# Kernel tuning notes

Measured on AMD Instinct MI355X. Metric: run time of the kernel, lower is better.

Reference implementation:

```python
import jax, jax.numpy as jnp
import numpy as np

N_NODES = 100000
NODES_PER_GRAPH = 200
N_GRAPHS = N_NODES // NODES_PER_GRAPH  # 500
N_EDGES = 3200000
NUM_FEATURES = 128
HIDDEN = 32
K_POOL = 50
NUM_CLASSES = 10
NUM_ITERATIONS = 3


def setup_inputs() -> dict:
    key = jax.random.key(0)
    ks = jax.random.split(key, 12)
    x = jax.random.normal(ks[0], (N_NODES, NUM_FEATURES), dtype=jnp.float32)
    edge_index = jax.random.randint(ks[1], (2, N_EDGES), 0, N_NODES, dtype=jnp.int64)
    batch = (jnp.arange(N_NODES, dtype=jnp.int64) // NODES_PER_GRAPH)
    # GCN weights (glorot-ish scale) + biases
    W1 = jax.random.normal(ks[2], (NUM_FEATURES, HIDDEN), dtype=jnp.float32) * (1.0 / np.sqrt(NUM_FEATURES))
    b1 = jnp.zeros((HIDDEN,), dtype=jnp.float32)
    W2 = jax.random.normal(ks[3], (HIDDEN, HIDDEN), dtype=jnp.float32) * (1.0 / np.sqrt(HIDDEN))
    b2 = jnp.zeros((HIDDEN,), dtype=jnp.float32)
    W3 = jax.random.normal(ks[4], (HIDDEN, HIDDEN), dtype=jnp.float32) * (1.0 / np.sqrt(HIDDEN))
    b3 = jnp.zeros((HIDDEN,), dtype=jnp.float32)
    # Capsule weights: [out_capsules, in_capsules, out_length, in_length]
    Wc1 = jax.random.normal(ks[5], (16, K_POOL, 32, 3 * HIDDEN), dtype=jnp.float32) * 0.05
    Wc2 = jax.random.normal(ks[6], (NUM_CLASSES, 16, 16, 32), dtype=jnp.float32) * 0.05
    return {"x": x, "edge_index": edge_index, "batch": batch,
            "W1": W1, "b1": b1, "W2": W2, "b2": b2, "W3": W3, "b3": b3,
            "Wc1": Wc1, "Wc2": Wc2}


def _gcn_conv(x, W, b, src, dst, mask):
    # PyG GCNConv: remove self-loops already done (mask), add self-loops, sym-normalize.
    h = x @ W  # [N, H]
    deg = jnp.zeros((x.shape[0],), dtype=h.dtype).at[dst].add(mask) + 1.0  # self-loop adds 1
    dinv = jax.lax.rsqrt(deg)
    norm = dinv[src] * dinv[dst] * mask  # [E]
    agg = jnp.zeros_like(h).at[dst].add(norm[:, None] * h[src])
    agg = agg + h * (dinv * dinv)[:, None]  # self-loop contribution h_i / deg_i
    return agg + b


def _squash(s, axis=-1):
    sq = jnp.sum(s * s, axis=axis, keepdims=True)
    return (sq / (1.0 + sq)) * s * jax.lax.rsqrt(sq + 1e-12)


def _capsule_linear(u, W, num_iterations):
    # u: [B, I, in_len]; W: [O, I, out_len, in_len]
    priors = jnp.einsum('oiLl,bil->boiL', W, u)  # [B, O, I, out_len]
    logits = jnp.zeros(priors.shape[:3] + (1,), dtype=priors.dtype)
    for it in range(num_iterations):
        c = jax.nn.softmax(logits, axis=1)             # over out capsules
        s = jnp.sum(c * priors, axis=2)                # [B, O, out_len]
        v = _squash(s)
        if it < num_iterations - 1:
            logits = logits + jnp.sum(priors * v[:, :, None, :], axis=-1, keepdims=True)
    return v


def _global_sort_pool(x, k):
    # x: [N, C], equal-size graphs -> [B, nper, C]; sort desc by last channel, take top-k
    xg = x.reshape(N_GRAPHS, NODES_PER_GRAPH, x.shape[-1])
    order = jnp.argsort(-xg[:, :, -1], axis=1)[:, :k]  # [B, k]
    return jnp.take_along_axis(xg, order[:, :, None], axis=1)  # [B, k, C]


def reference(x, edge_index, batch, W1, b1, W2, b2, W3, b3, Wc1, Wc2):
    src, dst = edge_index[0], edge_index[1]
    mask = (src != dst).astype(x.dtype)  # remove_self_loops
    x1 = jnp.tanh(_gcn_conv(x, W1, b1, src, dst, mask))
    x2 = jnp.tanh(_gcn_conv(x1, W2, b2, src, dst, mask))
    x3 = jnp.tanh(_gcn_conv(x2, W3, b3, src, dst, mask))
    xc = jnp.concatenate([x1, x2, x3], axis=-1)        # [N, 96]
    pooled = _global_sort_pool(xc, K_POOL)             # [B, 50, 96]
    out = _capsule_linear(pooled, Wc1, NUM_ITERATIONS)  # [B, 16, 32]
    out = _capsule_linear(out, Wc2, NUM_ITERATIONS)     # [B, 10, 16]
    return jnp.linalg.norm(out, axis=-1)                # [B, 10]
```

## Files before the change

kernel.cpp:

```cpp
#include <hip/hip_runtime.h>

#define NNODES 100000
#define NEDGES 3200000
#define NPG 200
#define NGRAPH 500
#define FIN 128
#define HID 32
#define KP 50
#define NCLS 10

#define NB1 196
#define BSH 9
#define CHUNK 8192
#define NBLK1 391
#define CAP 17408

__global__ __launch_bounds__(512) void k_place1(const int* __restrict__ src,
                                                const int* __restrict__ dst,
                                                int* __restrict__ cursor,
                                                unsigned* __restrict__ csorted) {
    __shared__ int hist[NB1];
    __shared__ int lstart[NB1];
    __shared__ int base[NB1];
    __shared__ int cnt2[NB1];
    __shared__ int sarr[256];
    __shared__ unsigned buf[CHUNK];
    __shared__ int dbuf[CHUNK];
    int t = threadIdx.x;
    for (int i = t; i < NB1; i += 512) { hist[i] = 0; cnt2[i] = 0; }
    __syncthreads();
    int eb = blockIdx.x * CHUNK;
    for (int i = 0; i < CHUNK / 512; ++i) {
        int e = eb + t + i * 512;
        if (e < NEDGES) {
            int s = src[e], d = dst[e];
            if (s != d) atomicAdd(&hist[d >> BSH], 1);
        }
    }
    __syncthreads();
    if (t < 256) sarr[t] = (t < NB1) ? hist[t] : 0;
    __syncthreads();
    for (int ofs = 1; ofs < 256; ofs <<= 1) {
        int add = (t < 256 && t >= ofs) ? sarr[t - ofs] : 0;
        __syncthreads();
        if (t < 256) sarr[t] += add;
        __syncthreads();
    }
    if (t < NB1) {
        lstart[t] = (t == 0) ? 0 : sarr[t - 1];
        base[t] = hist[t] ? (t * CAP + atomicAdd(&cursor[t], hist[t])) : 0;
    }
    __syncthreads();
    for (int i = 0; i < CHUNK / 512; ++i) {
        int e = eb + t + i * 512;
        if (e < NEDGES) {
            int s = src[e], d = dst[e];
            if (s != d) {
                int bk = d >> BSH;
                int pos = atomicAdd(&cnt2[bk], 1);
                int slot = lstart[bk] + pos;
                buf[slot] = ((unsigned)s << BSH) | (unsigned)(d & 511);
                dbuf[slot] = base[bk] + pos;
            }
        }
    }
    __syncthreads();
    int nval = sarr[NB1 - 1];
    for (int j = t; j < nval; j += 512) csorted[dbuf[j]] = buf[j];
}

__global__ __launch_bounds__(512) void k_fill2(const int* __restrict__ cursor,
                                               const unsigned* __restrict__ csorted,
                                               int* __restrict__ csrc,
                                               int2* __restrict__ begend,
                                               float* __restrict__ dinv) {
    __shared__ int cnt[512];
    __shared__ int loffs[512];
    __shared__ int cnt2[512];
    __shared__ int sarr[512];
    int b = blockIdx.x, t = threadIdx.x;
    cnt[t] = 0; cnt2[t] = 0;
    __syncthreads();
    int base = b * CAP;
    int m = cursor[b];
    for (int j = t; j < m; j += 512) atomicAdd(&cnt[csorted[base + j] & 511], 1);
    __syncthreads();
    sarr[t] = cnt[t];
    __syncthreads();
    for (int ofs = 1; ofs < 512; ofs <<= 1) {
        int add = (t >= ofs) ? sarr[t - ofs] : 0;
        __syncthreads();
        sarr[t] += add;
        __syncthreads();
    }
    loffs[t] = sarr[t] - cnt[t];
    __syncthreads();
    int n = b * 512 + t;
    if (n < NNODES) {
        int beg = base + loffs[t];
        begend[n] = make_int2(beg, beg + cnt[t]);
        dinv[n] = rsqrtf((float)cnt[t] + 1.0f);
    }
    for (int j = t; j < m; j += 512) {
        unsigned p = csorted[base + j];
        int d = p & 511;
        int pos = atomicAdd(&cnt2[d], 1);
        csrc[base + loffs[d] + pos] = (int)(p >> BSH);
    }
}

__global__ __launch_bounds__(256) void k_matmul(const float* __restrict__ X, int ldx, int K,
                                                const float* __restrict__ W,
                                                const float* __restrict__ dinv,
                                                float* __restrict__ h) {
    __shared__ float Xl[64 * FIN];
    __shared__ float Wqf[(FIN / 4) * 128];
    int t = threadIdx.x;
    for (int idx = t; idx < K * HID; idx += 256) {
        int k = idx >> 5, j = idx & 31;
        Wqf[(k >> 2) * 128 + j * 4 + (k & 3)] = W[idx];
    }
    int n0 = blockIdx.x * 64;
    int ng = 64 * K / 4;
    for (int idx = t; idx < ng; idx += 256) {
        int r = (idx * 4) / K, c = (idx * 4) % K;
        float4 v = make_float4(0.f, 0.f, 0.f, 0.f);
        if (n0 + r < NNODES)
            v = *reinterpret_cast<const float4*>(X + (size_t)(n0 + r) * ldx + c);
        *reinterpret_cast<float4*>(&Xl[r * K + c]) = v;
    }
    __syncthreads();
    int j = t & 31, g = t >> 5;
    const float* xr = &Xl[(g * 8) * K];
    const float4* wq = reinterpret_cast<const float4*>(Wqf);
    float a[8] = {0, 0, 0, 0, 0, 0, 0, 0};
    int K4 = K >> 2;
    for (int k4 = 0; k4 < K4; ++k4) {
        float4 wv = wq[k4 * 32 + j];
#pragma unroll
        for (int r = 0; r < 8; ++r) {
            float4 xv = *reinterpret_cast<const float4*>(&xr[r * K + k4 * 4]);
            a[r] += xv.x * wv.x + xv.y * wv.y + xv.z * wv.z + xv.w * wv.w;
        }
    }
    int r0 = n0 + g * 8;
#pragma unroll
    for (int q = 0; q < 8; ++q)
        if (r0 + q < NNODES) h[(size_t)(r0 + q) * HID + j] = a[q] * dinv[r0 + q];
}

__global__ __launch_bounds__(256) void k_gather(const int2* __restrict__ begend,
                                                const int* __restrict__ csrc,
                                                const float* __restrict__ dinv,
                                                const float* __restrict__ hw,
                                                const float* __restrict__ bias,
                                                float* __restrict__ xc, int coloff) {
    int t = threadIdx.x;
    int wv = t >> 6;
    int lane = t & 63;
    int nh = lane >> 5;
    int sub = lane & 31;
    int g = sub >> 3;
    int q = sub & 7;
    int n = blockIdx.x * 8 + wv * 2 + nh;
    int2 be = begend[n];
    int beg = be.x, end = be.y, last = end - 1;
    float4 acc = make_float4(0.f, 0.f, 0.f, 0.f);
    for (int e0 = beg + g; e0 < end; e0 += 32) {
#pragma unroll
        for (int j = 0; j < 8; ++j) {
            int e = e0 + 4 * j;
            float mk = (e <= last) ? 1.f : 0.f;
            int s = csrc[min(e, last)];
            float4 hv = *reinterpret_cast<const float4*>(hw + (size_t)s * HID + q * 4);
            acc.x += mk * hv.x; acc.y += mk * hv.y; acc.z += mk * hv.z; acc.w += mk * hv.w;
        }
    }
    for (int m = 8; m <= 16; m <<= 1) {
        acc.x += __shfl_xor(acc.x, m, 64);
        acc.y += __shfl_xor(acc.y, m, 64);
        acc.z += __shfl_xor(acc.z, m, 64);
        acc.w += __shfl_xor(acc.w, m, 64);
    }
    if (g == 0) {
        float di = dinv[n];
        float4 hv = *reinterpret_cast<const float4*>(hw + (size_t)n * HID + q * 4);
        float4 bv = *reinterpret_cast<const float4*>(bias + q * 4);
        float4 v;
        v.x = tanhf(di * (acc.x + hv.x) + bv.x);
        v.y = tanhf(di * (acc.y + hv.y) + bv.y);
        v.z = tanhf(di * (acc.z + hv.z) + bv.z);
        v.w = tanhf(di * (acc.w + hv.w) + bv.w);
        *reinterpret_cast<float4*>(xc + (size_t)n * 96 + coloff + q * 4) = v;
    }
}

__global__ __launch_bounds__(256) void k_sortpool(const float* __restrict__ xc,
                                                  float* __restrict__ pooled) {
    int g = blockIdx.x;
    __shared__ float vals[NPG];
    __shared__ int sel[KP];
    int t = threadIdx.x;
    if (t < NPG) vals[t] = xc[((size_t)g * NPG + t) * 96 + 95];
    __syncthreads();
    if (t < NPG) {
        float v = vals[t];
        int r = 0;
        for (int k = 0; k < NPG; ++k) {
            float vk = vals[k];
            r += (vk > v) || (vk == v && k < t);
        }
        if (r < KP) sel[r] = t;
    }
    __syncthreads();
    for (int idx = t; idx < KP * 24; idx += 256) {
        int r = idx / 24, c4 = (idx % 24) * 4;
        *reinterpret_cast<float4*>(pooled + (size_t)g * KP * 96 + r * 96 + c4) =
            *reinterpret_cast<const float4*>(xc + ((size_t)g * NPG + sel[r]) * 96 + c4);
    }
}

__global__ __launch_bounds__(512, 2) void k_priors1(const float* __restrict__ pooled,
                                                    const float* __restrict__ Wc1,
                                                    float* __restrict__ priors) {
    int bid = blockIdx.x;
    int ct = bid & 3;
    int bt = (bid >> 2) & 1;
    int i = bid >> 3;
    __shared__ float As[48 * 256];
    __shared__ float Bs[48 * 128];
    int t = threadIdx.x;
    int tx = t & 15, ty = t >> 4;
    float acc[8][8];
#pragma unroll
    for (int r = 0; r < 8; ++r)
#pragma unroll
        for (int c = 0; c < 8; ++c) acc[r][c] = 0.f;

    for (int kh = 0; kh < 2; ++kh) {
        int kbase = kh * 48;
        __syncthreads();
        for (int idx = t; idx < 256 * 12; idx += 512) {
            int r = idx / 12, c4 = (idx % 12) * 4;
            int b = bt * 256 + r;
            float4 v = make_float4(0.f, 0.f, 0.f, 0.f);
            if (b < NGRAPH)
                v = *reinterpret_cast<const float4*>(pooled + ((size_t)b * KP + i) * 96 + kbase + c4);
            float vv[4] = {v.x, v.y, v.z, v.w};
#pragma unroll
            for (int j = 0; j < 4; ++j) {
                int k = c4 + j;
                int gp = (r >> 2) ^ ((k >> 2) & 31);
                As[k * 256 + gp * 4 + (r & 3)] = vv[j];
            }
        }
        for (int idx = t; idx < 128 * 12; idx += 512) {
            int c = idx / 12, c4 = (idx % 12) * 4;
            int col = ct * 128 + c;
            const float* wr = Wc1 + (((size_t)(col >> 5) * KP + i) * 32 + (col & 31)) * 96;
            float4 v = *reinterpret_cast<const float4*>(wr + kbase + c4);
            float vv[4] = {v.x, v.y, v.z, v.w};
#pragma unroll
            for (int j = 0; j < 4; ++j) {
                int k = c4 + j;
                int gp = (c >> 2) ^ ((k >> 2) & 31);
                Bs[k * 128 + gp * 4 + (c & 3)] = vv[j];
            }
        }
        __syncthreads();
        for (int k = 0; k < 48; ++k) {
            int key = (k >> 2) & 31;
            float4 a0 = *reinterpret_cast<const float4*>(&As[k * 256 + 4 * (ty ^ key)]);
            float4 a1 = *reinterpret_cast<const float4*>(&As[k * 256 + 4 * ((32 + ty) ^ key)]);
            float4 b0 = *reinterpret_cast<const float4*>(&Bs[k * 128 + 4 * (tx ^ key)]);
            float4 b1 = *reinterpret_cast<const float4*>(&Bs[k * 128 + 4 * ((16 + tx) ^ key)]);
            float a[8] = {a0.x, a0.y, a0.z, a0.w, a1.x, a1.y, a1.z, a1.w};
            float bb[8] = {b0.x, b0.y, b0.z, b0.w, b1.x, b1.y, b1.z, b1.w};
#pragma unroll
            for (int r = 0; r < 8; ++r)
#pragma unroll
                for (int c = 0; c < 8; ++c) acc[r][c] += a[r] * bb[c];
        }
    }
#pragma unroll
    for (int rh = 0; rh < 2; ++rh)
#pragma unroll
        for (int rr = 0; rr < 4; ++rr) {
            int b = bt * 256 + rh * 128 + ty * 4 + rr;
            if (b >= NGRAPH) continue;
#pragma unroll
            for (int ch = 0; ch < 2; ++ch) {
                int col = ct * 128 + ch * 64 + tx * 4;
                int o = col >> 5, L = col & 31;
                float4 v = make_float4(acc[rh * 4 + rr][ch * 4 + 0],
                                       acc[rh * 4 + rr][ch * 4 + 1],
                                       acc[rh * 4 + rr][ch * 4 + 2],
                                       acc[rh * 4 + rr][ch * 4 + 3]);
                *reinterpret_cast<float4*>(priors + (((size_t)b * 16 + o) * KP + i) * 32 + L) = v;
            }
        }
}

__global__ __launch_bounds__(256) void k_routing1(const float* __restrict__ priors_g,
                                                  float* __restrict__ v_out) {
    int b = blockIdx.x;
    __shared__ float P[16 * KP * 33];
    __shared__ float logits[16 * KP];
    __shared__ float c[16 * KP];
    __shared__ float s[16 * 32];
    __shared__ float v[16 * 32];
    __shared__ float scale[16];
    int t = threadIdx.x;
    const float* pg = priors_g + (size_t)b * (16 * KP * 32);
    for (int idx = t; idx < 16 * KP * 32; idx += 256)
        P[(idx >> 5) * 33 + (idx & 31)] = pg[idx];
    for (int idx = t; idx < 16 * KP; idx += 256) logits[idx] = 0.f;
    __syncthreads();
    for (int it = 0; it < 3; ++it) {
        if (t < KP) {
            float m = -1e30f;
            for (int o = 0; o < 16; ++o) m = fmaxf(m, logits[o * KP + t]);
            float sum = 0.f;
            for (int o = 0; o < 16; ++o) {
                float e = expf(logits[o * KP + t] - m);
                c[o * KP + t] = e;
                sum += e;
            }
            for (int o = 0; o < 16; ++o) c[o * KP + t] /= sum;
        }
        __syncthreads();
        for (int idx = t; idx < 16 * 32; idx += 256) {
            int o = idx >> 5, L = idx & 31;
            float acc = 0.f;
            for (int i = 0; i < KP; ++i) acc += c[o * KP + i] * P[(o * KP + i) * 33 + L];
            s[idx] = acc;
        }
        __syncthreads();
        if (t < 16) {
            float sq = 0.f;
            for (int L = 0; L < 32; ++L) sq += s[t * 32 + L] * s[t * 32 + L];
            scale[t] = (sq / (1.f + sq)) * (1.0f / sqrtf(sq + 1e-12f));
        }
        __syncthreads();
        for (int idx = t; idx < 16 * 32; idx += 256) v[idx] = s[idx] * scale[idx >> 5];
        __syncthreads();
        if (it < 2) {
            for (int idx = t; idx < 16 * KP; idx += 256) {
                int o = idx / KP, i = idx % KP;
                float acc = 0.f;
                for (int L = 0; L < 32; ++L) acc += P[(o * KP + i) * 33 + L] * v[o * 32 + L];
                logits[idx] += acc;
            }
            __syncthreads();
        }
    }
    for (int idx = t; idx < 16 * 32; idx += 256) v_out[(size_t)b * 512 + idx] = v[idx];
}

__global__ __launch_bounds__(256) void k_caps2(const float* __restrict__ v1,
                                               const float* __restrict__ Wc2,
                                               float* __restrict__ out) {
    int b = blockIdx.x;
    __shared__ float ul[16 * 32];
    __shared__ float P[NCLS * 16 * 17];
    __shared__ float logits[NCLS * 16];
    __shared__ float c[NCLS * 16];
    __shared__ float s[NCLS * 16];
    __shared__ float v[NCLS * 16];
    __shared__ float scale[NCLS];
    int t = threadIdx.x;
    for (int idx = t; idx < 512; idx += 256) ul[idx] = v1[(size_t)b * 512 + idx];
    for (int idx = t; idx < NCLS * 16; idx += 256) logits[idx] = 0.f;
    __syncthreads();
    for (int idx = t; idx < NCLS * 16 * 16; idx += 256) {
        int L = idx & 15, i = (idx >> 4) & 15, o = idx >> 8;
        const float4* wr = reinterpret_cast<const float4*>(Wc2 + ((size_t)((o * 16 + i) * 16 + L)) * 32);
        const float4* ur = reinterpret_cast<const float4*>(&ul[i * 32]);
        float acc = 0.f;
#pragma unroll
        for (int l = 0; l < 8; ++l) {
            float4 w4 = wr[l], u4 = ur[l];
            acc += w4.x * u4.x + w4.y * u4.y + w4.z * u4.z + w4.w * u4.w;
        }
        P[(idx >> 4) * 17 + L] = acc;
    }
    __syncthreads();
    for (int it = 0; it < 3; ++it) {
        if (t < 16) {
            float m = -1e30f;
            for (int o = 0; o < NCLS; ++o) m = fmaxf(m, logits[o * 16 + t]);
            float sum = 0.f;
            for (int o = 0; o < NCLS; ++o) {
                float e = expf(logits[o * 16 + t] - m);
                c[o * 16 + t] = e;
                sum += e;
            }
            for (int o = 0; o < NCLS; ++o) c[o * 16 + t] /= sum;
        }
        __syncthreads();
        if (t < NCLS * 16) {
            int o = t >> 4, L = t & 15;
            float acc = 0.f;
            for (int i = 0; i < 16; ++i) acc += c[o * 16 + i] * P[(o * 16 + i) * 17 + L];
            s[t] = acc;
        }
        __syncthreads();
        if (t < NCLS) {
            float sq = 0.f;
            for (int L = 0; L < 16; ++L) sq += s[t * 16 + L] * s[t * 16 + L];
            scale[t] = (sq / (1.f + sq)) * (1.0f / sqrtf(sq + 1e-12f));
        }
        __syncthreads();
        if (t < NCLS * 16) v[t] = s[t] * scale[t >> 4];
        __syncthreads();
        if (it < 2) {
            if (t < NCLS * 16) {
                int o = t >> 4, i = t & 15;
                float acc = 0.f;
                for (int L = 0; L < 16; ++L) acc += P[(o * 16 + i) * 17 + L] * v[o * 16 + L];
                logits[t] += acc;
            }
            __syncthreads();
        }
    }
    if (t < NCLS) {
        float sq = 0.f;
        for (int L = 0; L < 16; ++L) sq += v[t * 16 + L] * v[t * 16 + L];
        out[(size_t)b * NCLS + t] = sqrtf(sq);
    }
}

extern "C" void kernel_launch(void* const* d_in, const int* in_sizes, int n_in,
                              void* d_out, int out_size, void* d_ws, size_t ws_size,
                              hipStream_t stream) {
    const float* x   = (const float*)d_in[0];
    const int*   ei  = (const int*)d_in[1];
    const float* W1  = (const float*)d_in[3];
    const float* b1  = (const float*)d_in[4];
    const float* W2  = (const float*)d_in[5];
    const float* b2  = (const float*)d_in[6];
    const float* W3  = (const float*)d_in[7];
    const float* b3  = (const float*)d_in[8];
    const float* Wc1 = (const float*)d_in[9];
    const float* Wc2 = (const float*)d_in[10];
    float* out = (float*)d_out;
    float* wsf = (float*)d_ws;

    const int* src = ei;
    const int* dst = ei + NEDGES;

    float* xc = wsf;
    float* R  = wsf + 9600000;
    int*   cursor  = (int*)R;
    float* dinv    = R + 256;
    int2*  begend  = (int2*)(R + 100256);
    float* A       = R + 300256;
    unsigned* csorted = (unsigned*)A;
    float* h       = A;
    float* pooled  = A;
    int*   csrc    = (int*)(R + 3712224);
    float* pr1     = R + 7124192;
    float* v1      = R + 19924192;

    hipMemsetAsync(cursor, 0, 256 * sizeof(int), stream);
    k_place1<<<NBLK1, 512, 0, stream>>>(src, dst, cursor, csorted);
    k_fill2<<<NB1, 512, 0, stream>>>(cursor, csorted, csrc, begend, dinv);

    k_matmul<<<(NNODES + 63) / 64, 256, 0, stream>>>(x, FIN, FIN, W1, dinv, h);
    k_gather<<<NNODES / 8, 256, 0, stream>>>(begend, csrc, dinv, h, b1, xc, 0);
    k_matmul<<<(NNODES + 63) / 64, 256, 0, stream>>>(xc, 96, HID, W2, dinv, h);
    k_gather<<<NNODES / 8, 256, 0, stream>>>(begend, csrc, dinv, h, b2, xc, 32);
    k_matmul<<<(NNODES + 63) / 64, 256, 0, stream>>>(xc + 32, 96, HID, W3, dinv, h);
    k_gather<<<NNODES / 8, 256, 0, stream>>>(begend, csrc, dinv, h, b3, xc, 64);

    k_sortpool<<<NGRAPH, 256, 0, stream>>>(xc, pooled);
    k_priors1<<<KP * 8, 512, 0, stream>>>(pooled, Wc1, pr1);
    k_routing1<<<NGRAPH, 256, 0, stream>>>(pr1, v1);
    k_caps2<<<NGRAPH, 256, 0, stream>>>(v1, Wc2, out);
}
```

Baseline: 383.7 us.

## Retile node-feature matmul as 256-row K-chunked outer-product GEMM with swizzled LDS

Rewrites the dense X@W kernel to process 256 rows per block in 32-wide K chunks, storing X transposed in LDS with an XOR swizzle and giving each thread an 8x4 register tile of outer-product accumulations. The old version kept all of a 64-row tile in LDS and did one dot product per output, which costs more LDS reads per FMA and uses a large LDS footprint. The new layout raises arithmetic intensity per LDS load and writes outputs as float4. In exchange there are 4x fewer blocks and an extra barrier per K chunk.

```diff
diff --git a/kernel.cpp b/kernel.cpp
--- a/kernel.cpp
+++ b/kernel.cpp
@@ -113,40 +113,67 @@
                                                 const float* __restrict__ W,
                                                 const float* __restrict__ dinv,
                                                 float* __restrict__ h) {
-    __shared__ float Xl[64 * FIN];
-    __shared__ float Wqf[(FIN / 4) * 128];
-    int t = threadIdx.x;
-    for (int idx = t; idx < K * HID; idx += 256) {
-        int k = idx >> 5, j = idx & 31;
-        Wqf[(k >> 2) * 128 + j * 4 + (k & 3)] = W[idx];
-    }
-    int n0 = blockIdx.x * 64;
-    int ng = 64 * K / 4;
-    for (int idx = t; idx < ng; idx += 256) {
-        int r = (idx * 4) / K, c = (idx * 4) % K;
-        float4 v = make_float4(0.f, 0.f, 0.f, 0.f);
-        if (n0 + r < NNODES)
-            v = *reinterpret_cast<const float4*>(X + (size_t)(n0 + r) * ldx + c);
-        *reinterpret_cast<float4*>(&Xl[r * K + c]) = v;
-    }
-    __syncthreads();
-    int j = t & 31, g = t >> 5;
-    const float* xr = &Xl[(g * 8) * K];
-    const float4* wq = reinterpret_cast<const float4*>(Wqf);
-    float a[8] = {0, 0, 0, 0, 0, 0, 0, 0};
-    int K4 = K >> 2;
-    for (int k4 = 0; k4 < K4; ++k4) {
-        float4 wv = wq[k4 * 32 + j];
-#pragma unroll
-        for (int r = 0; r < 8; ++r) {
-            float4 xv = *reinterpret_cast<const float4*>(&xr[r * K + k4 * 4]);
-            a[r] += xv.x * wv.x + xv.y * wv.y + xv.z * wv.z + xv.w * wv.w;
-        }
-    }
-    int r0 = n0 + g * 8;
-#pragma unroll
-    for (int q = 0; q < 8; ++q)
-        if (r0 + q < NNODES) h[(size_t)(r0 + q) * HID + j] = a[q] * dinv[r0 + q];
+    __shared__ float Xk[32 * 256];
+    __shared__ float Wl[32 * 36];
+    int t = threadIdx.x;
+    int tx = t & 7;
+    int ty = t >> 3;
+    int n0 = blockIdx.x * 256;
+    float acc[8][4];
+#pragma unroll
+    for (int r = 0; r < 8; ++r)
+#pragma unroll
+        for (int c = 0; c < 4; ++c) acc[r][c] = 0.f;
+
+    int ksteps = K >> 5;
+    for (int ks = 0; ks < ksteps; ++ks) {
+        int kbase = ks << 5;
+        __syncthreads();
+        for (int idx = t; idx < 256 * 8; idx += 256) {
+            int row = idx >> 3, c4 = (idx & 7) * 4;
+            float4 v = make_float4(0.f, 0.f, 0.f, 0.f);
+            if (n0 + row < NNODES)
+                v = *reinterpret_cast<const float4*>(X + (size_t)(n0 + row) * ldx + kbase + c4);
+            float vv[4] = {v.x, v.y, v.z, v.w};
+#pragma unroll
+            for (int j = 0; j < 4; ++j) {
+                int k = c4 + j;
+                int gp = (row >> 2) ^ ((k >> 2) & 31);
+                Xk[k * 256 + gp * 4 + (row & 3)] = vv[j];
+            }
+        }
+        for (int idx = t; idx < 32 * 32; idx += 256) {
+            int k = idx >> 5, j = idx & 31;
+            Wl[k * 36 + j] = W[(size_t)(kbase + k) * HID + j];
+        }
+        __syncthreads();
+        const float4* Xq = reinterpret_cast<const float4*>(Xk);
+        const float4* Wq = reinterpret_cast<const float4*>(Wl);
+        for (int k = 0; k < 32; ++k) {
+            int key = (k >> 2) & 31;
+            float4 a0 = Xq[k * 64 + (ty ^ key)];
+            float4 a1 = Xq[k * 64 + 32 + (ty ^ key)];
+            float4 wv = Wq[k * 9 + tx];
+            float a[8] = {a0.x, a0.y, a0.z, a0.w, a1.x, a1.y, a1.z, a1.w};
+#pragma unroll
+            for (int r = 0; r < 8; ++r) {
+                acc[r][0] += a[r] * wv.x;
+                acc[r][1] += a[r] * wv.y;
+                acc[r][2] += a[r] * wv.z;
+                acc[r][3] += a[r] * wv.w;
+            }
+        }
+    }
+#pragma unroll
+    for (int r = 0; r < 8; ++r) {
+        int row = (r < 4) ? (4 * ty + r) : (128 + 4 * ty + (r - 4));
+        int gr = n0 + row;
+        if (gr < NNODES) {
+            float di = dinv[gr];
+            float4 v = make_float4(acc[r][0] * di, acc[r][1] * di, acc[r][2] * di, acc[r][3] * di);
+            *reinterpret_cast<float4*>(h + (size_t)gr * HID + 4 * tx) = v;
+        }
+    }
 }
 
 __global__ __launch_bounds__(256) void k_gather(const int2* __restrict__ begend,
@@ -466,11 +493,11 @@
     k_place1<<<NBLK1, 512, 0, stream>>>(src, dst, cursor, csorted);
     k_fill2<<<NB1, 512, 0, stream>>>(cursor, csorted, csrc, begend, dinv);
 
-    k_matmul<<<(NNODES + 63) / 64, 256, 0, stream>>>(x, FIN, FIN, W1, dinv, h);
+    k_matmul<<<(NNODES + 255) / 256, 256, 0, stream>>>(x, FIN, FIN, W1, dinv, h);
     k_gather<<<NNODES / 8, 256, 0, stream>>>(begend, csrc, dinv, h, b1, xc, 0);
-    k_matmul<<<(NNODES + 63) / 64, 256, 0, stream>>>(xc, 96, HID, W2, dinv, h);
+    k_matmul<<<(NNODES + 255) / 256, 256, 0, stream>>>(xc, 96, HID, W2, dinv, h);
     k_gather<<<NNODES / 8, 256, 0, stream>>>(begend, csrc, dinv, h, b2, xc, 32);
-    k_matmul<<<(NNODES + 63) / 64, 256, 0, stream>>>(xc + 32, 96, HID, W3, dinv, h);
+    k_matmul<<<(NNODES + 255) / 256, 256, 0, stream>>>(xc + 32, 96, HID, W3, dinv, h);
     k_gather<<<NNODES / 8, 256, 0, stream>>>(begend, csrc, dinv, h, b3, xc, 64);
 
     k_sortpool<<<NGRAPH, 256, 0, stream>>>(xc, pooled);
```

Measured after the change: 372.2 us. 3.0% less time.
